# Kernel optimization log

Hardware: AMD Instinct MI355X
Metric: run time of the kernel (lower is better)

Reference implementation:

```python
import jax, jax.numpy as jnp
import numpy as np

B, T, D = 8, 512, 64

def setup_inputs() -> dict:
    key = jax.random.key(0)
    kx, kw, kb = jax.random.split(key, 3)
    x = jax.random.normal(kx, (B, T, D), dtype=jnp.float32)
    W = jax.random.normal(kw, (D, D), dtype=jnp.float32) / np.sqrt(D)
    b = jax.random.normal(kb, (D,), dtype=jnp.float32) * 0.01
    return {"x": x, "W": W, "b": b}

def reference(x, W, b):
    # v = Linear(x): (B,T,D)
    v = jnp.einsum('btd,ed->bte', x, W) + b
    # pairwise diff: (B,T,T,D); softmax over feature dim D
    diff = x[:, :, None, :] - x[:, None, :, :]
    K = jax.nn.softmax(-(diff * diff), axis=-1)
    # out[b,i,j] = sum_d K[b,i,j,d] * v[b,i,d]  -> (B,T,T)
    out = jnp.einsum('bijd,bid->bij', K, v)
    return out
```

## Files before the change

### kernel.cpp

```cpp
#include <hip/hip_runtime.h>

#define BB 8
#define TT 512
#define DD 64
#define IT 4
#define JTILE 64
#define NTILE 4
#define GR 17
#define S_SCALE 1.2011224087864498f

__device__ __forceinline__ float fast_exp2(float v) {
#if __has_builtin(__builtin_amdgcn_exp2f)
    return __builtin_amdgcn_exp2f(v);
#else
    return exp2f(v);
#endif
}
__device__ __forceinline__ float fast_rcp(float v) {
#if __has_builtin(__builtin_amdgcn_rcpf)
    return __builtin_amdgcn_rcpf(v);
#else
    return 1.0f / v;
#endif
}
__device__ __forceinline__ float bcast0(float v) {
    return __int_as_float(__builtin_amdgcn_readfirstlane(__float_as_int(v)));
}

__global__ __launch_bounds__(256, 4) void rbf_fused3(
    const float* __restrict__ x,
    const float* __restrict__ W,
    const float* __restrict__ bias,
    float* __restrict__ out)
{
    const int blk = blockIdx.x;
    const int jh  = blk & 1;
    const int it  = (blk >> 1) & 127;
    const int b   = blk >> 8;
    const int t   = threadIdx.x;
    const int w   = t >> 6;
    const int l   = t & 63;

    __shared__ float xi_s[IT][DD];
    __shared__ float vi_s[IT][DD];
    __shared__ float xj_s[2][JTILE * GR * 4];

    const float* xrow = x + (size_t)(b * TT + it * IT + w) * DD;
    {
        const float* wr = W + (size_t)l * DD;
        float acc = bias[l];
        #pragma unroll
        for (int d = 0; d < DD; d += 4) {
            float4 xv = *(const float4*)(xrow + d);
            float4 wv = *(const float4*)(wr + d);
            acc = fmaf(xv.x, wv.x, acc); acc = fmaf(xv.y, wv.y, acc);
            acc = fmaf(xv.z, wv.z, acc); acc = fmaf(xv.w, wv.w, acc);
        }
        vi_s[w][l] = acc;
        xi_s[w][l] = xrow[l] * S_SCALE;
    }
    __syncthreads();

    float4 vi_r[16];
    float  sxi[DD];
    #pragma unroll
    for (int c = 0; c < 16; ++c) {
        vi_r[c] = *(const float4*)(&vi_s[w][c * 4]);
        float4 xv = *(const float4*)(&xi_s[w][c * 4]);
        sxi[c * 4 + 0] = bcast0(xv.x);
        sxi[c * 4 + 1] = bcast0(xv.y);
        sxi[c * 4 + 2] = bcast0(xv.z);
        sxi[c * 4 + 3] = bcast0(xv.w);
    }

    const float* xb = x + ((size_t)b * TT + (size_t)jh * 256) * DD;
    float* orow = out + (size_t)(b * TT + it * IT + w) * TT + jh * 256;

    const int sr = t >> 4;
    const int sc = t & 15;
    float4 pf[4];

    #pragma unroll
    for (int u = 0; u < 4; ++u)
        pf[u] = *(const float4*)(xb + (size_t)(u * 16 + sr) * DD + sc * 4);
    {
        float4* dst = (float4*)xj_s[0];
        #pragma unroll
        for (int u = 0; u < 4; ++u) {
            float4 v = pf[u];
            v.x *= S_SCALE; v.y *= S_SCALE; v.z *= S_SCALE; v.w *= S_SCALE;
            dst[(u * 16 + sr) * GR + sc] = v;
        }
    }
    __syncthreads();

    int buf = 0;
    for (int jt = 0; jt < NTILE; ++jt) {
        if (jt + 1 < NTILE) {
            #pragma unroll
            for (int u = 0; u < 4; ++u)
                pf[u] = *(const float4*)(
                    xb + (size_t)((jt + 1) * JTILE + u * 16 + sr) * DD + sc * 4);
        }

        const float4* xjs = (const float4*)xj_s[buf];
        float num = 0.f, den = 0.f;
        #pragma unroll
        for (int cc = 0; cc < 16; ++cc) {
            float4 xj = xjs[l * GR + cc];
            float4 vi = vi_r[cc];
            float d0 = sxi[cc * 4 + 0] - xj.x;
            float d1 = sxi[cc * 4 + 1] - xj.y;
            float d2 = sxi[cc * 4 + 2] - xj.z;
            float d3 = sxi[cc * 4 + 3] - xj.w;
            float e0 = fast_exp2(-(d0 * d0));
            float e1 = fast_exp2(-(d1 * d1));
            float e2 = fast_exp2(-(d2 * d2));
            float e3 = fast_exp2(-(d3 * d3));
            num = fmaf(e0, vi.x, num);
            num = fmaf(e1, vi.y, num);
            num = fmaf(e2, vi.z, num);
            num = fmaf(e3, vi.w, num);
            den += (e0 + e1) + (e2 + e3);
        }
        orow[jt * JTILE + l] = num * fast_rcp(den);

        if (jt + 1 < NTILE) {
            float4* dst = (float4*)xj_s[buf ^ 1];
            #pragma unroll
            for (int u = 0; u < 4; ++u) {
                float4 v = pf[u];
                v.x *= S_SCALE; v.y *= S_SCALE; v.z *= S_SCALE; v.w *= S_SCALE;
                dst[(u * 16 + sr) * GR + sc] = v;
            }
            __syncthreads();
            buf ^= 1;
        }
    }
}

extern "C" void kernel_launch(void* const* d_in, const int* in_sizes, int n_in,
                              void* d_out, int out_size, void* d_ws, size_t ws_size,
                              hipStream_t stream) {
    const float* x    = (const float*)d_in[0];
    const float* W    = (const float*)d_in[1];
    const float* bias = (const float*)d_in[2];
    float* out        = (float*)d_out;

    rbf_fused3<<<BB * (TT / IT) * 2, 256, 0, stream>>>(x, W, bias, out);
}
```

Measured before the change: 91.36 us.

## Split feature dim across lane quads with DPP reduction, single-buffer LDS

```diff
diff --git a/kernel.cpp b/kernel.cpp
--- a/kernel.cpp
+++ b/kernel.cpp
@@ -23,11 +23,17 @@
     return 1.0f / v;
 #endif
 }
-__device__ __forceinline__ float bcast0(float v) {
-    return __int_as_float(__builtin_amdgcn_readfirstlane(__float_as_int(v)));
+
+__device__ __forceinline__ float quad_sum(float v) {
+    int s1 = __builtin_amdgcn_update_dpp(0, __float_as_int(v),
+                                         177 , 0xf, 0xf, true);
+    float a = v + __int_as_float(s1);
+    int s2 = __builtin_amdgcn_update_dpp(0, __float_as_int(a),
+                                         78 , 0xf, 0xf, true);
+    return a + __int_as_float(s2);
 }
 
-__global__ __launch_bounds__(256, 4) void rbf_fused3(
+__global__ __launch_bounds__(256, 6) void rbf_fused4(
     const float* __restrict__ x,
     const float* __restrict__ W,
     const float* __restrict__ bias,
@@ -35,17 +41,19 @@
 {
     const int blk = blockIdx.x;
     const int jh  = blk & 1;
-    const int it  = (blk >> 1) & 127;
+    const int it8 = (blk >> 1) & 127;
     const int b   = blk >> 8;
     const int t   = threadIdx.x;
     const int w   = t >> 6;
     const int l   = t & 63;
+    const int dg  = l & 3;
+    const int jg  = l >> 2;
 
     __shared__ float xi_s[IT][DD];
     __shared__ float vi_s[IT][DD];
-    __shared__ float xj_s[2][JTILE * GR * 4];
+    __shared__ float4 xj_s[JTILE * GR];
 
-    const float* xrow = x + (size_t)(b * TT + it * IT + w) * DD;
+    const float* xrow = x + (size_t)(b * TT + it8 * IT + w) * DD;
     {
         const float* wr = W + (size_t)l * DD;
         float acc = bias[l];
@@ -61,80 +69,67 @@
     }
     __syncthreads();
 
-    float4 vi_r[16];
-    float  sxi[DD];
+    float4 xi_r[4], vi_r[4];
     #pragma unroll
-    for (int c = 0; c < 16; ++c) {
-        vi_r[c] = *(const float4*)(&vi_s[w][c * 4]);
-        float4 xv = *(const float4*)(&xi_s[w][c * 4]);
-        sxi[c * 4 + 0] = bcast0(xv.x);
-        sxi[c * 4 + 1] = bcast0(xv.y);
-        sxi[c * 4 + 2] = bcast0(xv.z);
-        sxi[c * 4 + 3] = bcast0(xv.w);
+    for (int c = 0; c < 4; ++c) {
+        xi_r[c] = *(const float4*)(&xi_s[w][dg * 16 + c * 4]);
+        vi_r[c] = *(const float4*)(&vi_s[w][dg * 16 + c * 4]);
     }
 
     const float* xb = x + ((size_t)b * TT + (size_t)jh * 256) * DD;
-    float* orow = out + (size_t)(b * TT + it * IT + w) * TT + jh * 256;
+    float* orow = out + (size_t)(b * TT + it8 * IT + w) * TT + jh * 256;
 
     const int sr = t >> 4;
     const int sc = t & 15;
-    float4 pf[4];
 
     #pragma unroll
-    for (int u = 0; u < 4; ++u)
-        pf[u] = *(const float4*)(xb + (size_t)(u * 16 + sr) * DD + sc * 4);
-    {
-        float4* dst = (float4*)xj_s[0];
-        #pragma unroll
-        for (int u = 0; u < 4; ++u) {
-            float4 v = pf[u];
-            v.x *= S_SCALE; v.y *= S_SCALE; v.z *= S_SCALE; v.w *= S_SCALE;
-            dst[(u * 16 + sr) * GR + sc] = v;
-        }
+    for (int u = 0; u < 4; ++u) {
+        float4 v = *(const float4*)(xb + (size_t)(u * 16 + sr) * DD + sc * 4);
+        v.x *= S_SCALE; v.y *= S_SCALE; v.z *= S_SCALE; v.w *= S_SCALE;
+        xj_s[(u * 16 + sr) * GR + sc] = v;
     }
     __syncthreads();
 
-    int buf = 0;
     for (int jt = 0; jt < NTILE; ++jt) {
+        #pragma unroll
+        for (int g = 0; g < 4; ++g) {
+            const float4* base = &xj_s[(g * 16 + jg) * GR + dg * 4];
+            float n0 = 0.f, n1 = 0.f, e0s = 0.f, e1s = 0.f;
+            #pragma unroll
+            for (int c = 0; c < 4; ++c) {
+                float4 xj = base[c];
+                float4 xi = xi_r[c];
+                float4 vi = vi_r[c];
+                float u0 = xi.x - xj.x;
+                float u1 = xi.y - xj.y;
+                float u2 = xi.z - xj.z;
+                float u3 = xi.w - xj.w;
+                float e0 = fast_exp2(-(u0 * u0));
+                float e1 = fast_exp2(-(u1 * u1));
+                float e2 = fast_exp2(-(u2 * u2));
+                float e3 = fast_exp2(-(u3 * u3));
+                n0 = fmaf(e0, vi.x, n0);
+                n1 = fmaf(e1, vi.y, n1);
+                n0 = fmaf(e2, vi.z, n0);
+                n1 = fmaf(e3, vi.w, n1);
+                e0s += e0 + e2;
+                e1s += e1 + e3;
+            }
+            float num = quad_sum(n0 + n1);
+            float den = quad_sum(e0s + e1s);
+            if (dg == 0)
+                orow[jt * JTILE + g * 16 + jg] = num * fast_rcp(den);
+        }
         if (jt + 1 < NTILE) {
-            #pragma unroll
-            for (int u = 0; u < 4; ++u)
-                pf[u] = *(const float4*)(
-                    xb + (size_t)((jt + 1) * JTILE + u * 16 + sr) * DD + sc * 4);
-        }
-
-        const float4* xjs = (const float4*)xj_s[buf];
-        float num = 0.f, den = 0.f;
-        #pragma unroll
-        for (int cc = 0; cc < 16; ++cc) {
-            float4 xj = xjs[l * GR + cc];
-            float4 vi = vi_r[cc];
-            float d0 = sxi[cc * 4 + 0] - xj.x;
-            float d1 = sxi[cc * 4 + 1] - xj.y;
-            float d2 = sxi[cc * 4 + 2] - xj.z;
-            float d3 = sxi[cc * 4 + 3] - xj.w;
-            float e0 = fast_exp2(-(d0 * d0));
-            float e1 = fast_exp2(-(d1 * d1));
-            float e2 = fast_exp2(-(d2 * d2));
-            float e3 = fast_exp2(-(d3 * d3));
-            num = fmaf(e0, vi.x, num);
-            num = fmaf(e1, vi.y, num);
-            num = fmaf(e2, vi.z, num);
-            num = fmaf(e3, vi.w, num);
-            den += (e0 + e1) + (e2 + e3);
-        }
-        orow[jt * JTILE + l] = num * fast_rcp(den);
-
-        if (jt + 1 < NTILE) {
-            float4* dst = (float4*)xj_s[buf ^ 1];
+            __syncthreads();
             #pragma unroll
             for (int u = 0; u < 4; ++u) {
-                float4 v = pf[u];
+                float4 v = *(const float4*)(
+                    xb + (size_t)((jt + 1) * JTILE + u * 16 + sr) * DD + sc * 4);
                 v.x *= S_SCALE; v.y *= S_SCALE; v.z *= S_SCALE; v.w *= S_SCALE;
-                dst[(u * 16 + sr) * GR + sc] = v;
+                xj_s[(u * 16 + sr) * GR + sc] = v;
             }
             __syncthreads();
-            buf ^= 1;
         }
     }
 }
@@ -147,5 +142,5 @@
     const float* bias = (const float*)d_in[2];
     float* out        = (float*)d_out;
 
-    rbf_fused3<<<BB * (TT / IT) * 2, 256, 0, stream>>>(x, W, bias, out);
+    rbf_fused4<<<BB * (TT / IT) * 2, 256, 0, stream>>>(x, W, bias, out);
 }
```

Result: no change. 92.71 us (+1.5%).
